# Optimization experiments

Measured on AMD Instinct MI355X. Metric: run time of the kernel, lower is better.

Reference implementation:

```python
import jax, jax.numpy as jnp
import numpy as np

B, S, D, H = 2, 2048, 1024, 16
HD = D // H
SCALE = HD ** -0.5

def setup_inputs() -> dict:
    key = jax.random.key(0)
    ks = jax.random.split(key, 5)
    x = jax.random.normal(ks[0], (B, S, D), dtype=jnp.float32)
    Wqkv = jax.random.normal(ks[1], (D, 3 * D), dtype=jnp.float32) * (D ** -0.5)
    bqkv = jnp.zeros((3 * D,), dtype=jnp.float32)
    Wproj = jax.random.normal(ks[2], (D, D), dtype=jnp.float32) * (D ** -0.5)
    bproj = jnp.zeros((D,), dtype=jnp.float32)
    return {"x": x, "Wqkv": Wqkv, "bqkv": bqkv, "Wproj": Wproj, "bproj": bproj}

def reference(x, Wqkv, bqkv, Wproj, bproj):
    b, s, _ = x.shape
    qkv = x @ Wqkv + bqkv                       # [B,S,3D]
    qkv = qkv.reshape(b, s, 3, H, HD)
    q, k, v = [jnp.transpose(qkv[:, :, i], (0, 2, 1, 3)) for i in range(3)]  # [B,H,S,HD]
    attn = jnp.einsum('bhqd,bhkd->bhqk', q, k) * SCALE   # [B,H,S,S]
    attn = jax.nn.softmax(attn, axis=-1)
    out = jnp.einsum('bhqk,bhkd->bhqd', attn, v)         # [B,H,S,HD]
    out = jnp.transpose(out, (0, 2, 1, 3)).reshape(b, s, D)
    return out @ Wproj + bproj
```

## Files before the change

### kernel.cpp

```cpp
#include <hip/hip_runtime.h>
#include <hip/hip_bf16.h>

#define BB 2
#define SS 2048
#define DD 1024
#define HH 16
#define HDD 64
#define MM (BB*SS)
#define NQKV (3*DD)
#define SCALE 0.125f
#define QPRESCALE 0.18033688f

typedef __bf16 bf16_t;
typedef bf16_t bf16x4 __attribute__((ext_vector_type(4)));
typedef bf16_t bf16x8 __attribute__((ext_vector_type(8)));
typedef float f32x4 __attribute__((ext_vector_type(4)));
typedef float f32x16 __attribute__((ext_vector_type(16)));

__device__ __forceinline__ void gl_lds16(const bf16_t* g, bf16_t* l) {
    __builtin_amdgcn_global_load_lds(
        (const __attribute__((address_space(1))) unsigned int*)(uintptr_t)g,
        (__attribute__((address_space(3))) unsigned int*)(uintptr_t)l,
        16, 0, 0);
}

__device__ __forceinline__ f32x4 MF(bf16x8 a, bf16x8 b, f32x4 c) {
    return __builtin_amdgcn_mfma_f32_16x16x32_bf16(a, b, c, 0, 0, 0);
}

__global__ __launch_bounds__(256) void prep(
    const float* __restrict__ x, const float* __restrict__ Wqkv,
    const float* __restrict__ Wproj, bf16_t* __restrict__ xb,
    bf16_t* __restrict__ wqkvt, bf16_t* __restrict__ wprojt)
{
    const int bx = blockIdx.x;
    if (bx < 2048) {
        int i = (bx * 256 + threadIdx.x) * 8;
        float4 a = *(const float4*)(x + i);
        float4 b = *(const float4*)(x + i + 4);
        bf16x8 v;
        v[0]=(bf16_t)a.x; v[1]=(bf16_t)a.y; v[2]=(bf16_t)a.z; v[3]=(bf16_t)a.w;
        v[4]=(bf16_t)b.x; v[5]=(bf16_t)b.y; v[6]=(bf16_t)b.z; v[7]=(bf16_t)b.w;
        *reinterpret_cast<bf16x8*>(xb + i) = v;
        return;
    }
    __shared__ float tile[32][33];
    const float* src; bf16_t* dst; int C, bxl, byl;
    if (bx < 5120) {
        int t = bx - 2048;
        byl = t / 96; bxl = t - byl * 96;
        src = Wqkv;  dst = wqkvt;  C = NQKV;
    } else {
        int t = bx - 5120;
        byl = t >> 5; bxl = t & 31;
        src = Wproj; dst = wprojt; C = DD;
    }
    const int R = DD;
    const int tx = threadIdx.x & 31, ty = threadIdx.x >> 5;
    const int r0 = byl * 32, c0 = bxl * 32;
    #pragma unroll
    for (int i = 0; i < 32; i += 8)
        tile[ty + i][tx] = src[(size_t)(r0 + ty + i) * C + c0 + tx];
    __syncthreads();
    #pragma unroll
    for (int i = 0; i < 32; i += 8)
        dst[(size_t)(c0 + ty + i) * R + r0 + tx] = (bf16_t)tile[tx][ty + i];
}

__global__ __launch_bounds__(512, 2) void gemm_qkv(
    const bf16_t* __restrict__ A, const bf16_t* __restrict__ Bt,
    const float* __restrict__ bias,
    bf16_t* __restrict__ qw, bf16_t* __restrict__ kw, bf16_t* __restrict__ vtw)
{
    constexpr int K  = DD;
    constexpr int BM = 256, BN = 192, BK = 64;
    constexpr int NT = K / BK;

    __shared__ __align__(16) bf16_t smem[2 * BM * BK + 2 * BN * BK];
    bf16_t* const As0 = smem;
    bf16_t* const As1 = smem + BM * BK;
    bf16_t* const Bs0 = smem + 2 * BM * BK;
    bf16_t* const Bs1 = Bs0 + BN * BK;

    const int tid  = threadIdx.x;
    const int w    = tid >> 6;
    const int lane = tid & 63;
    const int lr   = lane & 15;
    const int quad = lane >> 4;
    const int wm   = w >> 2;
    const int wn   = w & 3;
    const int m0   = blockIdx.y * BM;
    const int n0   = blockIdx.x * BN;

    const int sx   = lr & 7;
    const int ecc0 = ((quad)     ^ sx) * 8;
    const int ecc1 = ((quad + 4) ^ sx) * 8;
    const int aOff = (wm * 128 + lr) * BK;
    const int bOff = (wn * 48  + lr) * BK;

    f32x4 acc[2][4][3];
    #pragma unroll
    for (int mh = 0; mh < 2; mh++)
        #pragma unroll
        for (int mi = 0; mi < 4; mi++)
            #pragma unroll
            for (int ni = 0; ni < 3; ni++)
                acc[mh][mi][ni] = (f32x4){0.f, 0.f, 0.f, 0.f};

    auto stageA = [&](int kt, bf16_t* dst) {
        #pragma unroll
        for (int r = 0; r < 4; ++r) {
            const int c   = r * 512 + tid;
            const int row = c >> 3;
            const int cg  = (c & 7) ^ (row & 7);
            gl_lds16(A + (size_t)(m0 + row) * K + kt * BK + cg * 8, dst + c * 8);
        }
    };
    auto stageB = [&](int kt, bf16_t* dst) {
        #pragma unroll
        for (int r = 0; r < 3; ++r) {
            const int c   = r * 512 + tid;
            const int row = c >> 3;
            const int cg  = (c & 7) ^ (row & 7);
            gl_lds16(Bt + (size_t)(n0 + row) * K + kt * BK + cg * 8, dst + c * 8);
        }
    };

    stageA(0, As0);
    stageB(0, Bs0);
    asm volatile("s_waitcnt vmcnt(0)" ::: "memory");
    __builtin_amdgcn_s_barrier();

    auto tile = [&](int t, const bf16_t* Ac, const bf16_t* Bc,
                    bf16_t* An, bf16_t* Bn) {
        const bool more = (t + 1) < NT;
        bf16x8 af[8], bk[3];

        #pragma unroll
        for (int mi = 0; mi < 4; mi++) {
            af[mi]     = *(const bf16x8*)(Ac + aOff + mi * 16 * BK + ecc0);
            af[4 + mi] = *(const bf16x8*)(Ac + aOff + (64 + mi * 16) * BK + ecc0);
        }
        #pragma unroll
        for (int ni = 0; ni < 3; ni++)
            bk[ni] = *(const bf16x8*)(Bc + bOff + ni * 16 * BK + ecc0);
        if (more) { stageA(t + 1, An); stageB(t + 1, Bn); }
        __builtin_amdgcn_s_barrier();
        __builtin_amdgcn_sched_barrier(0);
        __builtin_amdgcn_s_setprio(1);
        #pragma unroll
        for (int mh = 0; mh < 2; mh++)
            #pragma unroll
            for (int mi = 0; mi < 4; mi++)
                #pragma unroll
                for (int ni = 0; ni < 3; ni++)
                    acc[mh][mi][ni] = MF(af[mh * 4 + mi], bk[ni], acc[mh][mi][ni]);
        __builtin_amdgcn_s_setprio(0);
        __builtin_amdgcn_sched_barrier(0);

        #pragma unroll
        for (int mi = 0; mi < 4; mi++) {
            af[mi]     = *(const bf16x8*)(Ac + aOff + mi * 16 * BK + ecc1);
            af[4 + mi] = *(const bf16x8*)(Ac + aOff + (64 + mi * 16) * BK + ecc1);
        }
        #pragma unroll
        for (int ni = 0; ni < 3; ni++)
            bk[ni] = *(const bf16x8*)(Bc + bOff + ni * 16 * BK + ecc1);
        __builtin_amdgcn_s_barrier();
        __builtin_amdgcn_sched_barrier(0);
        __builtin_amdgcn_s_setprio(1);
        #pragma unroll
        for (int mh = 0; mh < 2; mh++)
            #pragma unroll
            for (int mi = 0; mi < 4; mi++)
                #pragma unroll
                for (int ni = 0; ni < 3; ni++)
                    acc[mh][mi][ni] = MF(af[mh * 4 + mi], bk[ni], acc[mh][mi][ni]);
        __builtin_amdgcn_s_setprio(0);
        __builtin_amdgcn_sched_barrier(0);
        if (more) asm volatile("s_waitcnt vmcnt(0)" ::: "memory");
        __builtin_amdgcn_s_barrier();
    };

    #pragma unroll 1
    for (int tt = 0; tt < NT; tt += 2) {
        tile(tt,     As0, Bs0, As1, Bs1);
        tile(tt + 1, As1, Bs1, As0, Bs0);
    }

    __builtin_amdgcn_s_barrier();

    const int colBase = n0 + wn * 48;
    const int vbase   = (n0 < 2048) ? 2048 : n0;
    #pragma unroll
    for (int mh = 0; mh < 2; mh++) {
        #pragma unroll
        for (int ni = 0; ni < 3; ni++) {
            const int col = colBase + ni * 16 + lr;
            const float bcol = bias[col];
            const int which = col >> 10;
            const int d = col & 1023;
            const int h = d >> 6, hd = d & 63;
            #pragma unroll
            for (int mi = 0; mi < 4; mi++) {
                const int rl0 = wm * 128 + mh * 64 + mi * 16 + quad * 4;
                if (which == 0) {
                    #pragma unroll
                    for (int reg = 0; reg < 4; reg++) {
                        const int row = m0 + rl0 + reg;
                        const int b = row >> 11, s = row & 2047;
                        qw[(((size_t)(b * HH + h)) * SS + s) * HDD + hd] =
                            (bf16_t)((acc[mh][mi][ni][reg] + bcol) * QPRESCALE);
                    }
                } else if (which == 1) {
                    #pragma unroll
                    for (int reg = 0; reg < 4; reg++) {
                        const int row = m0 + rl0 + reg;
                        const int b = row >> 11, s = row & 2047;
                        kw[(((size_t)(b * HH + h)) * SS + s) * HDD + hd] =
                            (bf16_t)(acc[mh][mi][ni][reg] + bcol);
                    }
                } else {
                    bf16x4 pk;
                    #pragma unroll
                    for (int reg = 0; reg < 4; reg++)
                        pk[reg] = (bf16_t)(acc[mh][mi][ni][reg] + bcol);
                    const int lc = col - vbase;
                    *reinterpret_cast<bf16x4*>(&smem[lc * 264 + rl0]) = pk;
                }
            }
        }
    }
    const int nv = n0 + BN - 2048;
    if (nv > 0) {
        __builtin_amdgcn_s_barrier();
        const int nvc = nv < BN ? nv : BN;
        const int lcb = tid >> 5;
        const int rl  = (tid & 31) * 8;
        const int b   = m0 >> 11;
        const int s   = (m0 & 2047) + rl;
        for (int j = 0; j < nvc / 16; j++) {
            const int lc = j * 16 + lcb;
            bf16x8 vv = *reinterpret_cast<const bf16x8*>(&smem[lc * 264 + rl]);
            const int col = vbase + lc;
            const int d = col & 1023;
            const int h = d >> 6, hd = d & 63;
            *reinterpret_cast<bf16x8*>(
                vtw + (((size_t)(b * HH + h)) * HDD + hd) * SS + s) = vv;
        }
    }
}

__global__ __launch_bounds__(256) void gemm_bt64(
    const bf16_t* __restrict__ A, const bf16_t* __restrict__ Bt,
    const float* __restrict__ bias, float* __restrict__ outf, int N, int K)
{
    __shared__ __align__(16) bf16_t As[2][64 * 32];
    __shared__ __align__(16) bf16_t Bs[2][128 * 32];

    const int tid  = threadIdx.x;
    const int w    = tid >> 6;
    const int lane = tid & 63;
    const int lr   = lane & 15;
    const int quad = lane >> 4;
    const int m0   = blockIdx.y * 64;
    const int n0   = blockIdx.x * 128;
    const int wm   = w >> 1;
    const int wn   = w & 1;

    f32x4 acc[2][4];
    #pragma unroll
    for (int i = 0; i < 2; i++)
        #pragma unroll
        for (int j = 0; j < 4; j++) acc[i][j] = (f32x4){0.f, 0.f, 0.f, 0.f};

    const int stgRow = lane >> 2;
    const int stgCol = (lane & 3) * 8;
    const bf16_t* aPtr = A  + (size_t)(m0 + w * 16 + stgRow) * K + stgCol;
    const bf16_t* bPtr = Bt + (size_t)(n0 + w * 32 + stgRow) * K + stgCol;
    const size_t rowSkip = (size_t)16 * K;

    for (int ks = 0; ks < K; ks += 64) {
        __syncthreads();
        #pragma unroll
        for (int s = 0; s < 2; s++) {
            const int ko = ks + s * 32;
            gl_lds16(aPtr + ko,           &As[s][w * 512]);
            gl_lds16(bPtr + ko,           &Bs[s][w * 1024]);
            gl_lds16(bPtr + rowSkip + ko, &Bs[s][w * 1024 + 512]);
        }
        __syncthreads();

        #pragma unroll
        for (int s = 0; s < 2; s++) {
            bf16x8 af[2], bf[4];
            #pragma unroll
            for (int mi = 0; mi < 2; mi++)
                af[mi] = *reinterpret_cast<const bf16x8*>(&As[s][(wm * 32 + mi * 16 + lr) * 32 + quad * 8]);
            #pragma unroll
            for (int ni = 0; ni < 4; ni++)
                bf[ni] = *reinterpret_cast<const bf16x8*>(&Bs[s][(wn * 64 + ni * 16 + lr) * 32 + quad * 8]);
            #pragma unroll
            for (int mi = 0; mi < 2; mi++)
                #pragma unroll
                for (int ni = 0; ni < 4; ni++)
                    acc[mi][ni] = __builtin_amdgcn_mfma_f32_16x16x32_bf16(af[mi], bf[ni], acc[mi][ni], 0, 0, 0);
        }
    }

    #pragma unroll
    for (int mi = 0; mi < 2; mi++)
        #pragma unroll
        for (int ni = 0; ni < 4; ni++)
            #pragma unroll
            for (int reg = 0; reg < 4; reg++) {
                int row = m0 + wm * 32 + mi * 16 + quad * 4 + reg;
                int col = n0 + wn * 64 + ni * 16 + lr;
                outf[(size_t)row * N + col] = acc[mi][ni][reg] + bias[col];
            }
}

__global__ __launch_bounds__(512, 4) void attn_kernel(
    const bf16_t* __restrict__ qws, const bf16_t* __restrict__ kws,
    const bf16_t* __restrict__ vtws, bf16_t* __restrict__ ob)
{
    __shared__ __align__(16) bf16_t smem[34048];
    bf16_t* Ks = smem;
    bf16_t* Vs = smem + 16640;

    const int tid  = threadIdx.x;
    const int w    = tid >> 6;
    const int g    = w >> 2;
    const int wg   = w & 3;
    const int lane = tid & 63;
    const int ln31 = lane & 31;
    const int ln5  = lane >> 5;

    const int qb = blockIdx.x;
    const int bh = blockIdx.y;
    const int b  = bh >> 4;
    const int h  = bh & 15;

    const bf16_t* Qh  = qws  + (size_t)bh * SS * HDD;
    const bf16_t* Kh  = kws  + (size_t)bh * SS * HDD;
    const bf16_t* Vth = vtws + (size_t)bh * HDD * SS;

    const int q0w    = qb * 128 + wg * 32;
    const int kvbase = g * 1024;

    bf16x8 aq[4];
    #pragma unroll
    for (int f = 0; f < 4; f++)
        aq[f] = *(const bf16x8*)(Qh + (size_t)(q0w + ln31) * HDD + f * 16 + ln5 * 8);

    const int gtid = tid & 255;
    const int sc = gtid & 7;
    const int sr = gtid >> 3;

    {
        const int ko = g * 520;
        const int vo = g * 4352;
        bf16x8 k0 = *(const bf16x8*)(Kh  + (size_t)(kvbase + sr     ) * HDD + sc * 8);
        bf16x8 k1 = *(const bf16x8*)(Kh  + (size_t)(kvbase + sr + 32) * HDD + sc * 8);
        bf16x8 v0 = *(const bf16x8*)(Vth + (size_t)(sr     ) * SS + kvbase + sc * 8);
        bf16x8 v1 = *(const bf16x8*)(Vth + (size_t)(sr + 32) * SS + kvbase + sc * 8);
        *reinterpret_cast<bf16x8*>(&Ks[(ko + sc * 65 + sr     ) * 8]) = k0;
        *reinterpret_cast<bf16x8*>(&Ks[(ko + sc * 65 + sr + 32) * 8]) = k1;
        bf16_t* vd0 = &Vs[vo + (sr     ) * 68 + sc * 8];
        bf16_t* vd1 = &Vs[vo + (sr + 32) * 68 + sc * 8];
        *reinterpret_cast<bf16x4*>(vd0)     = __builtin_shufflevector(v0, v0, 0,1,2,3);
        *reinterpret_cast<bf16x4*>(vd0 + 4) = __builtin_shufflevector(v0, v0, 4,5,6,7);
        *reinterpret_cast<bf16x4*>(vd1)     = __builtin_shufflevector(v1, v1, 0,1,2,3);
        *reinterpret_cast<bf16x4*>(vd1 + 4) = __builtin_shufflevector(v1, v1, 4,5,6,7);
    }
    __syncthreads();

    float l = 0.f;
    f32x16 o[2];
    #pragma unroll
    for (int nh = 0; nh < 2; nh++)
        #pragma unroll
        for (int r = 0; r < 16; r++) o[nh][r] = 0.f;

    int buf = 0;
    for (int it = 0; it < 16; ++it) {
        const int ko = buf * 1040 + g * 520;
        const int vo = buf * 8704 + g * 4352;

        f32x16 sfr[2];
        #pragma unroll
        for (int ni = 0; ni < 2; ni++) {
            #pragma unroll
            for (int r = 0; r < 16; r++) sfr[ni][r] = 0.f;
            #pragma unroll
            for (int f = 0; f < 4; f++) {
                bf16x8 kb = *reinterpret_cast<const bf16x8*>(
                    &Ks[(ko + (2 * f + ln5) * 65 + ni * 32 + ln31) * 8]);
                sfr[ni] = __builtin_amdgcn_mfma_f32_32x32x16_bf16(kb, aq[f], sfr[ni], 0, 0, 0);
            }
        }

        bf16x8 nk0, nk1, nv0, nv1;
        const bool more = (it + 1 < 16);
        if (more) {
            const int kvn = kvbase + (it + 1) * 64;
            nk0 = *(const bf16x8*)(Kh  + (size_t)(kvn + sr     ) * HDD + sc * 8);
            nk1 = *(const bf16x8*)(Kh  + (size_t)(kvn + sr + 32) * HDD + sc * 8);
            nv0 = *(const bf16x8*)(Vth + (size_t)(sr     ) * SS + kvn + sc * 8);
            nv1 = *(const bf16x8*)(Vth + (size_t)(sr + 32) * SS + kvn + sc * 8);
        }

        float p[2][16];
        #pragma unroll
        for (int ni = 0; ni < 2; ni++)
            #pragma unroll
            for (int r = 0; r < 16; r++) {
                p[ni][r] = __builtin_amdgcn_exp2f(sfr[ni][r]);
                l += p[ni][r];
            }

        bf16x8 ap[4];
        #pragma unroll
        for (int c16 = 0; c16 < 4; c16++)
            #pragma unroll
            for (int j = 0; j < 8; j++)
                ap[c16][j] = (bf16_t)p[c16 >> 1][(c16 & 1) * 8 + j];

        #pragma unroll
        for (int nh = 0; nh < 2; nh++) {
            const bf16_t* vrow = &Vs[vo + (nh * 32 + ln31) * 68];
            #pragma unroll
            for (int c16 = 0; c16 < 4; c16++) {
                bf16x4 lo = *(const bf16x4*)(vrow + c16 * 16 + 4 * ln5);
                bf16x4 hi = *(const bf16x4*)(vrow + c16 * 16 + 8 + 4 * ln5);
                bf16x8 vb = __builtin_shufflevector(lo, hi, 0, 1, 2, 3, 4, 5, 6, 7);
                o[nh] = __builtin_amdgcn_mfma_f32_32x32x16_bf16(ap[c16], vb, o[nh], 0, 0, 0);
            }
        }

        if (more) {
            const int ko1 = (buf ^ 1) * 1040 + g * 520;
            const int vo1 = (buf ^ 1) * 8704 + g * 4352;
            *reinterpret_cast<bf16x8*>(&Ks[(ko1 + sc * 65 + sr     ) * 8]) = nk0;
            *reinterpret_cast<bf16x8*>(&Ks[(ko1 + sc * 65 + sr + 32) * 8]) = nk1;
            bf16_t* vd0 = &Vs[vo1 + (sr     ) * 68 + sc * 8];
            bf16_t* vd1 = &Vs[vo1 + (sr + 32) * 68 + sc * 8];
            *reinterpret_cast<bf16x4*>(vd0)     = __builtin_shufflevector(nv0, nv0, 0,1,2,3);
            *reinterpret_cast<bf16x4*>(vd0 + 4) = __builtin_shufflevector(nv0, nv0, 4,5,6,7);
            *reinterpret_cast<bf16x4*>(vd1)     = __builtin_shufflevector(nv1, nv1, 0,1,2,3);
            *reinterpret_cast<bf16x4*>(vd1 + 4) = __builtin_shufflevector(nv1, nv1, 4,5,6,7);
        }
        __syncthreads();
        buf ^= 1;
    }

    l += __shfl_xor(l, 32, 64);

    __syncthreads();
    float* Of = (float*)smem;
    float* Lf = (float*)(smem + 16384);
    if (ln5 == 0) Lf[g * 128 + wg * 32 + ln31] = l;
    if (g == 1) {
        #pragma unroll
        for (int nh = 0; nh < 2; nh++)
            #pragma unroll
            for (int r = 0; r < 16; r++) {
                const int q = (r & 3) + 8 * (r >> 2) + 4 * ln5;
                Of[(wg * 32 + q) * 64 + nh * 32 + ln31] = o[nh][r];
            }
    }
    __syncthreads();
    if (g == 0) {
        float inv[16];
        #pragma unroll
        for (int r = 0; r < 16; r++) {
            const int q = (r & 3) + 8 * (r >> 2) + 4 * ln5;
            inv[r] = 1.f / (Lf[wg * 32 + q] + Lf[128 + wg * 32 + q]);
        }
        #pragma unroll
        for (int nh = 0; nh < 2; nh++)
            #pragma unroll
            for (int r = 0; r < 16; r++) {
                const int q  = (r & 3) + 8 * (r >> 2) + 4 * ln5;
                const int hd = nh * 32 + ln31;
                float val = (o[nh][r] + Of[(wg * 32 + q) * 64 + hd]) * inv[r];
                ob[((size_t)b * SS + q0w + q) * DD + h * HDD + hd] = (bf16_t)val;
            }
    }
}

extern "C" void kernel_launch(void* const* d_in, const int* in_sizes, int n_in,
                              void* d_out, int out_size, void* d_ws, size_t ws_size,
                              hipStream_t stream) {
    const float* x     = (const float*)d_in[0];
    const float* Wqkv  = (const float*)d_in[1];
    const float* bqkv  = (const float*)d_in[2];
    const float* Wproj = (const float*)d_in[3];
    const float* bproj = (const float*)d_in[4];
    float* out = (float*)d_out;

    const size_t NEL = (size_t)MM * DD;
    bf16_t* qws    = (bf16_t*)d_ws;
    bf16_t* kws    = qws  + NEL;
    bf16_t* vtws   = kws  + NEL;
    bf16_t* xb     = vtws + NEL;
    bf16_t* ows    = xb;
    bf16_t* wqkvt  = xb + NEL;
    bf16_t* wprojt = wqkvt + (size_t)NQKV * DD;

    prep<<<6144, 256, 0, stream>>>(x, Wqkv, Wproj, xb, wqkvt, wprojt);

    gemm_qkv<<<dim3(NQKV / 192, MM / 256), 512, 0, stream>>>(
        xb, wqkvt, bqkv, qws, kws, vtws);

    attn_kernel<<<dim3(SS / 128, BB * HH), 512, 0, stream>>>(qws, kws, vtws, ows);

    gemm_bt64<<<dim3(DD / 128, MM / 64), 256, 0, stream>>>(
        ows, wprojt, bproj, out, DD, DD);
}
```

Before: 179.8 us.

## Triple-buffer QKV GEMM with BK=32, prefetch distance two, and block swizzle

Rewrites the QKV projection GEMM main loop. It halves the K tile to 32, rotates three LDS buffers, and prefetches two tiles ahead with partial vmcnt waits, so there is one barrier per step instead of a full drain every tile. It also remaps block indices so neighbouring workgroups share A/B tiles in L2, and drops the XOR LDS swizzle. The V-transpose staging stride changes from 264 to 260. The tradeoffs are possible LDS bank conflicts from the unswizzled layout, more barriers per unit of K, and 16-byte LDS reads that are no longer 16-byte aligned in the V staging path.

Result: no change. 179.4 us (-0.2%).

```diff
diff --git a/kernel.cpp b/kernel.cpp
--- a/kernel.cpp
+++ b/kernel.cpp
@@ -73,14 +73,12 @@
     bf16_t* __restrict__ qw, bf16_t* __restrict__ kw, bf16_t* __restrict__ vtw)
 {
     constexpr int K  = DD;
-    constexpr int BM = 256, BN = 192, BK = 64;
+    constexpr int BM = 256, BN = 192, BK = 32;
     constexpr int NT = K / BK;
 
-    __shared__ __align__(16) bf16_t smem[2 * BM * BK + 2 * BN * BK];
-    bf16_t* const As0 = smem;
-    bf16_t* const As1 = smem + BM * BK;
-    bf16_t* const Bs0 = smem + 2 * BM * BK;
-    bf16_t* const Bs1 = Bs0 + BN * BK;
+    __shared__ __align__(16) bf16_t smem[50176];
+    bf16_t* const Ab[3] = { smem, smem + 8192, smem + 16384 };
+    bf16_t* const Bb[3] = { smem + 24576, smem + 30720, smem + 36864 };
 
     const int tid  = threadIdx.x;
     const int w    = tid >> 6;
@@ -89,111 +87,84 @@
     const int quad = lane >> 4;
     const int wm   = w >> 2;
     const int wn   = w & 3;
-    const int m0   = blockIdx.y * BM;
-    const int n0   = blockIdx.x * BN;
-
-    const int sx   = lr & 7;
-    const int ecc0 = ((quad)     ^ sx) * 8;
-    const int ecc1 = ((quad + 4) ^ sx) * 8;
-    const int aOff = (wm * 128 + lr) * BK;
-    const int bOff = (wn * 48  + lr) * BK;
-
-    f32x4 acc[2][4][3];
-    #pragma unroll
-    for (int mh = 0; mh < 2; mh++)
-        #pragma unroll
-        for (int mi = 0; mi < 4; mi++)
+
+    const int flat = blockIdx.y * 16 + blockIdx.x;
+    const int swz  = (flat & 7) * 32 + (flat >> 3);
+    const int m0   = (swz >> 4) * BM;
+    const int n0   = (swz & 15) * BN;
+
+    f32x4 acc[8][3];
+    #pragma unroll
+    for (int mi = 0; mi < 8; mi++)
+        #pragma unroll
+        for (int ni = 0; ni < 3; ni++)
+            acc[mi][ni] = (f32x4){0.f, 0.f, 0.f, 0.f};
+
+    const int ca0 = tid,        ca1 = tid + 512;
+    const int cb0 = tid,        cb1 = tid + 256;
+    const bf16_t* aG0 = A  + (size_t)(m0 + (ca0 >> 2)) * K + (ca0 & 3) * 8;
+    const bf16_t* aG1 = A  + (size_t)(m0 + (ca1 >> 2)) * K + (ca1 & 3) * 8;
+    const bf16_t* bG0 = Bt + (size_t)(n0 + (cb0 >> 2)) * K + (cb0 & 3) * 8;
+    const bf16_t* bG1 = Bt + (size_t)(n0 + (cb1 >> 2)) * K + (cb1 & 3) * 8;
+
+    auto stage = [&](int kt, bf16_t* Ad, bf16_t* Bd) {
+        const int ko = kt * BK;
+        gl_lds16(aG0 + ko, Ad + ca0 * 8);
+        gl_lds16(aG1 + ko, Ad + ca1 * 8);
+        gl_lds16(bG0 + ko, Bd + cb0 * 8);
+        gl_lds16(bG1 + ko, Bd + cb1 * 8);
+    };
+
+    stage(0, Ab[0], Bb[0]);
+    stage(1, Ab[1], Bb[1]);
+    asm volatile("s_waitcnt vmcnt(4)" ::: "memory");
+    __builtin_amdgcn_s_barrier();
+    __builtin_amdgcn_sched_barrier(0);
+
+    const int aOff = (wm * 128 + lr) * BK + quad * 8;
+    const int bOff = (wn * 48  + lr) * BK + quad * 8;
+
+    auto tileStep = [&](int t, const bf16_t* Ac, const bf16_t* Bc,
+                        bf16_t* An, bf16_t* Bn) {
+        bf16x8 af[8], bk[3];
+        #pragma unroll
+        for (int mi = 0; mi < 8; mi++)
+            af[mi] = *(const bf16x8*)(Ac + aOff + mi * 16 * BK);
+        #pragma unroll
+        for (int ni = 0; ni < 3; ni++)
+            bk[ni] = *(const bf16x8*)(Bc + bOff + ni * 16 * BK);
+        if (t < NT - 2) stage(t + 2, An, Bn);
+        __builtin_amdgcn_sched_barrier(0);
+        __builtin_amdgcn_s_setprio(1);
+        #pragma unroll
+        for (int mi = 0; mi < 8; mi++)
             #pragma unroll
             for (int ni = 0; ni < 3; ni++)
-                acc[mh][mi][ni] = (f32x4){0.f, 0.f, 0.f, 0.f};
-
-    auto stageA = [&](int kt, bf16_t* dst) {
-        #pragma unroll
-        for (int r = 0; r < 4; ++r) {
-            const int c   = r * 512 + tid;
-            const int row = c >> 3;
-            const int cg  = (c & 7) ^ (row & 7);
-            gl_lds16(A + (size_t)(m0 + row) * K + kt * BK + cg * 8, dst + c * 8);
-        }
-    };
-    auto stageB = [&](int kt, bf16_t* dst) {
-        #pragma unroll
-        for (int r = 0; r < 3; ++r) {
-            const int c   = r * 512 + tid;
-            const int row = c >> 3;
-            const int cg  = (c & 7) ^ (row & 7);
-            gl_lds16(Bt + (size_t)(n0 + row) * K + kt * BK + cg * 8, dst + c * 8);
-        }
-    };
-
-    stageA(0, As0);
-    stageB(0, Bs0);
-    asm volatile("s_waitcnt vmcnt(0)" ::: "memory");
-    __builtin_amdgcn_s_barrier();
-
-    auto tile = [&](int t, const bf16_t* Ac, const bf16_t* Bc,
-                    bf16_t* An, bf16_t* Bn) {
-        const bool more = (t + 1) < NT;
-        bf16x8 af[8], bk[3];
-
-        #pragma unroll
-        for (int mi = 0; mi < 4; mi++) {
-            af[mi]     = *(const bf16x8*)(Ac + aOff + mi * 16 * BK + ecc0);
-            af[4 + mi] = *(const bf16x8*)(Ac + aOff + (64 + mi * 16) * BK + ecc0);
-        }
-        #pragma unroll
-        for (int ni = 0; ni < 3; ni++)
-            bk[ni] = *(const bf16x8*)(Bc + bOff + ni * 16 * BK + ecc0);
-        if (more) { stageA(t + 1, An); stageB(t + 1, Bn); }
+                acc[mi][ni] = MF(af[mi], bk[ni], acc[mi][ni]);
+        __builtin_amdgcn_s_setprio(0);
+        __builtin_amdgcn_sched_barrier(0);
+        if (t < NT - 2)       asm volatile("s_waitcnt vmcnt(4)" ::: "memory");
+        else if (t == NT - 2) asm volatile("s_waitcnt vmcnt(0)" ::: "memory");
         __builtin_amdgcn_s_barrier();
         __builtin_amdgcn_sched_barrier(0);
-        __builtin_amdgcn_s_setprio(1);
-        #pragma unroll
-        for (int mh = 0; mh < 2; mh++)
-            #pragma unroll
-            for (int mi = 0; mi < 4; mi++)
-                #pragma unroll
-                for (int ni = 0; ni < 3; ni++)
-                    acc[mh][mi][ni] = MF(af[mh * 4 + mi], bk[ni], acc[mh][mi][ni]);
-        __builtin_amdgcn_s_setprio(0);
-        __builtin_amdgcn_sched_barrier(0);
-
-        #pragma unroll
-        for (int mi = 0; mi < 4; mi++) {
-            af[mi]     = *(const bf16x8*)(Ac + aOff + mi * 16 * BK + ecc1);
-            af[4 + mi] = *(const bf16x8*)(Ac + aOff + (64 + mi * 16) * BK + ecc1);
-        }
-        #pragma unroll
-        for (int ni = 0; ni < 3; ni++)
-            bk[ni] = *(const bf16x8*)(Bc + bOff + ni * 16 * BK + ecc1);
-        __builtin_amdgcn_s_barrier();
-        __builtin_amdgcn_sched_barrier(0);
-        __builtin_amdgcn_s_setprio(1);
-        #pragma unroll
-        for (int mh = 0; mh < 2; mh++)
-            #pragma unroll
-            for (int mi = 0; mi < 4; mi++)
-                #pragma unroll
-                for (int ni = 0; ni < 3; ni++)
-                    acc[mh][mi][ni] = MF(af[mh * 4 + mi], bk[ni], acc[mh][mi][ni]);
-        __builtin_amdgcn_s_setprio(0);
-        __builtin_amdgcn_sched_barrier(0);
-        if (more) asm volatile("s_waitcnt vmcnt(0)" ::: "memory");
-        __builtin_amdgcn_s_barrier();
     };
 
     #pragma unroll 1
-    for (int tt = 0; tt < NT; tt += 2) {
-        tile(tt,     As0, Bs0, As1, Bs1);
-        tile(tt + 1, As1, Bs1, As0, Bs0);
-    }
+    for (int tt = 0; tt < NT - 2; tt += 3) {
+        tileStep(tt,     Ab[0], Bb[0], Ab[2], Bb[2]);
+        tileStep(tt + 1, Ab[1], Bb[1], Ab[0], Bb[0]);
+        tileStep(tt + 2, Ab[2], Bb[2], Ab[1], Bb[1]);
+    }
+    tileStep(NT - 2, Ab[0], Bb[0], nullptr, nullptr);
+    tileStep(NT - 1, Ab[1], Bb[1], nullptr, nullptr);
 
     __builtin_amdgcn_s_barrier();
 
     const int colBase = n0 + wn * 48;
     const int vbase   = (n0 < 2048) ? 2048 : n0;
     #pragma unroll
-    for (int mh = 0; mh < 2; mh++) {
+    for (int mi = 0; mi < 8; mi++) {
+        const int rl0 = wm * 128 + mi * 16 + quad * 4;
         #pragma unroll
         for (int ni = 0; ni < 3; ni++) {
             const int col = colBase + ni * 16 + lr;
@@ -201,33 +172,29 @@
             const int which = col >> 10;
             const int d = col & 1023;
             const int h = d >> 6, hd = d & 63;
-            #pragma unroll
-            for (int mi = 0; mi < 4; mi++) {
-                const int rl0 = wm * 128 + mh * 64 + mi * 16 + quad * 4;
-                if (which == 0) {
-                    #pragma unroll
-                    for (int reg = 0; reg < 4; reg++) {
-                        const int row = m0 + rl0 + reg;
-                        const int b = row >> 11, s = row & 2047;
-                        qw[(((size_t)(b * HH + h)) * SS + s) * HDD + hd] =
-                            (bf16_t)((acc[mh][mi][ni][reg] + bcol) * QPRESCALE);
-                    }
-                } else if (which == 1) {
-                    #pragma unroll
-                    for (int reg = 0; reg < 4; reg++) {
-                        const int row = m0 + rl0 + reg;
-                        const int b = row >> 11, s = row & 2047;
-                        kw[(((size_t)(b * HH + h)) * SS + s) * HDD + hd] =
-                            (bf16_t)(acc[mh][mi][ni][reg] + bcol);
-                    }
-                } else {
-                    bf16x4 pk;
-                    #pragma unroll
-                    for (int reg = 0; reg < 4; reg++)
-                        pk[reg] = (bf16_t)(acc[mh][mi][ni][reg] + bcol);
-                    const int lc = col - vbase;
-                    *reinterpret_cast<bf16x4*>(&smem[lc * 264 + rl0]) = pk;
+            if (which == 0) {
+                #pragma unroll
+                for (int reg = 0; reg < 4; reg++) {
+                    const int row = m0 + rl0 + reg;
+                    const int b = row >> 11, s = row & 2047;
+                    qw[(((size_t)(b * HH + h)) * SS + s) * HDD + hd] =
+                        (bf16_t)((acc[mi][ni][reg] + bcol) * QPRESCALE);
                 }
+            } else if (which == 1) {
+                #pragma unroll
+                for (int reg = 0; reg < 4; reg++) {
+                    const int row = m0 + rl0 + reg;
+                    const int b = row >> 11, s = row & 2047;
+                    kw[(((size_t)(b * HH + h)) * SS + s) * HDD + hd] =
+                        (bf16_t)(acc[mi][ni][reg] + bcol);
+                }
+            } else {
+                bf16x4 pk;
+                #pragma unroll
+                for (int reg = 0; reg < 4; reg++)
+                    pk[reg] = (bf16_t)(acc[mi][ni][reg] + bcol);
+                const int lc = col - vbase;
+                *reinterpret_cast<bf16x4*>(&smem[lc * 260 + rl0]) = pk;
             }
         }
     }
@@ -241,7 +208,7 @@
         const int s   = (m0 & 2047) + rl;
         for (int j = 0; j < nvc / 16; j++) {
             const int lc = j * 16 + lcb;
-            bf16x8 vv = *reinterpret_cast<const bf16x8*>(&smem[lc * 264 + rl]);
+            bf16x8 vv = *reinterpret_cast<const bf16x8*>(&smem[lc * 260 + rl]);
             const int col = vbase + lc;
             const int d = col & 1023;
             const int h = d >> 6, hd = d & 63;
```
